# Performance work log

Hardware: AMD Instinct MI355X
Metric: run time of the kernel (lower is better)

Reference implementation:

```python
import jax, jax.numpy as jnp
import numpy as np

K = 9
BN_EPS = 1e-5
NEG_SLOPE = 0.2


def setup_inputs() -> dict:
    key = jax.random.key(0)
    ks = jax.random.split(key, 8)
    B, C, H, W = 16, 128, 32, 32
    s1 = 1.0 / np.sqrt(2 * C)
    s2 = 1.0 / np.sqrt(C)
    return {
        "x": jax.random.normal(ks[0], (B, C, H, W), dtype=jnp.float32),
        "W1": jax.random.uniform(ks[1], (2 * C, C), dtype=jnp.float32, minval=-s1, maxval=s1),
        "b1": jax.random.uniform(ks[2], (C,), dtype=jnp.float32, minval=-s1, maxval=s1),
        "W2": jax.random.uniform(ks[3], (C, C), dtype=jnp.float32, minval=-s2, maxval=s2),
        "b2": jax.random.uniform(ks[4], (C,), dtype=jnp.float32, minval=-s2, maxval=s2),
        "gamma": jnp.ones((C,), dtype=jnp.float32),
        "beta": jnp.zeros((C,), dtype=jnp.float32),
    }


def _leaky_relu(h):
    return jnp.where(h >= 0, h, NEG_SLOPE * h)


def reference(x, W1, b1, W2, b2, gamma, beta):
    B, C, H, W = x.shape
    N = H * W
    r = x
    feats = x.reshape(B, C, N).transpose(0, 2, 1)  # (B, N, C)

    # pairwise squared Euclidean distances (ordering identical to torch.cdist p=2)
    sq = jnp.sum(feats * feats, axis=-1)  # (B, N)
    d2 = sq[:, :, None] + sq[:, None, :] - 2.0 * jnp.einsum("bnc,bmc->bnm", feats, feats)
    _, idx = jax.lax.top_k(-d2, K)  # k smallest distances -> (B, N, K) int32

    neighbors = jax.vmap(lambda f, i: f[i])(feats, idx)  # (B, N, K, C)
    center = feats[:, :, None, :]  # (B, N, 1, C)
    edge = jnp.concatenate(
        [jnp.broadcast_to(center, neighbors.shape), neighbors - center], axis=-1
    )  # (B, N, K, 2C)

    h = _leaky_relu(edge @ W1 + b1)
    h = h @ W2 + b2  # (B, N, K, C)
    msg = jnp.max(h, axis=2)  # (B, N, C)

    out = msg.transpose(0, 2, 1).reshape(B, C, H, W)

    # BatchNorm2d (training mode: batch statistics, biased variance)
    mean = jnp.mean(out, axis=(0, 2, 3), keepdims=True)
    var = jnp.mean((out - mean) ** 2, axis=(0, 2, 3), keepdims=True)
    g = gamma.reshape(1, C, 1, 1)
    b = beta.reshape(1, C, 1, 1)
    out = g * (out - mean) * jax.lax.rsqrt(var + BN_EPS) + b

    return jax.nn.relu(out + r)
```

## Files before the change

### kernel.cpp

```cpp
#include <hip/hip_runtime.h>

#define B_ 16
#define C_ 128
#define N_ 1024
#define K_ 9
#define NEG_SLOPE 0.2f
#define BN_EPS 1e-5f

typedef __attribute__((ext_vector_type(8))) short short8;
typedef __attribute__((ext_vector_type(4))) float f32x4;
typedef __attribute__((ext_vector_type(4))) unsigned short u16x4;

__device__ __forceinline__ unsigned short f2bf(float f) {
    union { float f; unsigned u; } v; v.f = f;
    unsigned r = v.u + 0x7fffu + ((v.u >> 16) & 1u);
    return (unsigned short)(r >> 16);
}
__device__ __forceinline__ float bf2f(unsigned short h) {
    union { unsigned u; float f; } v; v.u = ((unsigned)h) << 16; return v.f;
}
__device__ __forceinline__ unsigned umin_(unsigned a, unsigned b) { return a < b ? a : b; }

__global__ __launch_bounds__(256) void k_transpose(const float* __restrict__ x,
                                                   float* __restrict__ featsT)
{
    __shared__ float t[32][33];
    int blk = blockIdx.x;
    int b = blk / 128;
    int rem = blk % 128;
    int c0 = (rem / 32) * 32;
    int n0 = (rem % 32) * 32;
    int tj = threadIdx.x & 31;
    int ti = threadIdx.x >> 5;
    #pragma unroll
    for (int s = 0; s < 32; s += 8)
        t[ti + s][tj] = x[(b * C_ + c0 + ti + s) * N_ + n0 + tj];
    __syncthreads();
    #pragma unroll
    for (int s = 0; s < 32; s += 8)
        featsT[(b * N_ + n0 + ti + s) * C_ + c0 + tj] = t[tj][ti + s];
}

__global__ __launch_bounds__(256) void k_prep(const float* __restrict__ featsT,
        unsigned short* __restrict__ Bf, float* __restrict__ sq)
{
    int tid = threadIdx.x;
    int lane = tid & 63, wv = tid >> 6;
    int half = lane >> 5;
    int l2 = lane & 31;
    int gp = blockIdx.x * 8 + wv * 2 + half;
    int b = gp >> 10, n = gp & 1023;

    int ch0 = (l2 & 15) * 8;
    const float4* f4 = (const float4*)&featsT[gp * C_ + ch0];
    float4 v0 = f4[0], v1 = f4[1];

    u16x4 o0, o1;
    if (l2 < 16) {
        o0.x = f2bf(v0.x); o0.y = f2bf(v0.y); o0.z = f2bf(v0.z); o0.w = f2bf(v0.w);
        o1.x = f2bf(v1.x); o1.y = f2bf(v1.y); o1.z = f2bf(v1.z); o1.w = f2bf(v1.w);
    } else {
        o0.x = f2bf(v0.x - bf2f(f2bf(v0.x))); o0.y = f2bf(v0.y - bf2f(f2bf(v0.y)));
        o0.z = f2bf(v0.z - bf2f(f2bf(v0.z))); o0.w = f2bf(v0.w - bf2f(f2bf(v0.w)));
        o1.x = f2bf(v1.x - bf2f(f2bf(v1.x))); o1.y = f2bf(v1.y - bf2f(f2bf(v1.y)));
        o1.z = f2bf(v1.z - bf2f(f2bf(v1.z))); o1.w = f2bf(v1.w - bf2f(f2bf(v1.w)));
    }
    long chunk = (((long)(b * 8 + (l2 >> 2)) * 64 + (n >> 4)) << 6) + ((l2 & 3) * 16 + (n & 15));
    *(u16x4*)&Bf[chunk * 8]     = o0;
    *(u16x4*)&Bf[chunk * 8 + 4] = o1;

    float ss = v0.x*v0.x + v0.y*v0.y + v0.z*v0.z + v0.w*v0.w
             + v1.x*v1.x + v1.y*v1.y + v1.z*v1.z + v1.w*v1.w;
    #pragma unroll
    for (int off = 1; off < 16; off <<= 1)
        ss += __shfl_xor(ss, off);
    if (l2 == 0) sq[gp] = ss;
}

#define STAGE_READ(PH, VARR) do {                                              \
    const int tl_ = (PH) >> 1, rb_ = ((PH) & 1) * 2;                           \
    _Pragma("unroll")                                                          \
    for (int t = 0; t < 8; ++t) {                                              \
        int col = ((wv * 8 + t) << 4) + cl;                                    \
        keybuf[quad * 2 + 0][col] = karr[tl_][t][rb_ + 0];                     \
        keybuf[quad * 2 + 1][col] = karr[tl_][t][rb_ + 1];                     \
    }                                                                          \
    __syncthreads();                                                           \
    _Pragma("unroll")                                                          \
    for (int j = 0; j < 16; ++j) VARR[j] = keybuf[wv][lane + (j << 6)];        \
    __syncthreads();                                                           \
} while (0)

#define TOP2_INIT(VARR, M1, M2, J1, J2) do {                                   \
    M1 = 0xFFFFFFFFu; M2 = 0xFFFFFFFFu; J1 = 0; J2 = 0;                        \
    _Pragma("unroll")                                                          \
    for (int j = 0; j < 16; ++j) {                                             \
        unsigned x_ = VARR[j], jc_ = (unsigned)j;                              \
        bool b1_ = x_ < M1, b2_ = x_ < M2;                                     \
        unsigned tk_ = b1_ ? M1 : x_, tj_ = b1_ ? J1 : jc_;                    \
        M2 = b2_ ? tk_ : M2; J2 = b2_ ? tj_ : J2;                              \
        M1 = b1_ ? x_ : M1; J1 = b1_ ? jc_ : J1;                               \
    }                                                                          \
} while (0)

#define ROW_ROUND(VARR, M1, M2, J1, J2, G, ROWPTR) do {                        \
    bool t_ = (M1 == (G));                                                     \
    unsigned long long bal_ = __ballot(t_);                                    \
    bool win_;                                                                 \
    if (__popcll(bal_) > 1) {               \
        unsigned mc_ = t_ ? (unsigned)(lane + (J1 << 6)) : 0xFFFFFFFFu;        \
        unsigned cm_ = mc_;                                                    \
        _Pragma("unroll")                                                      \
        for (int off = 1; off < 64; off <<= 1)                                 \
            cm_ = umin_(cm_, (unsigned)__shfl_xor((int)cm_, off));             \
        win_ = t_ && (mc_ == cm_);                   \
    } else {                                                                   \
        win_ = t_;                                                             \
    }                                                                          \
    if (win_) {                                                                \
        idxout[(ROWPTR) + q] = lane + (int)(J1 << 6);                          \
        unsigned gk_ = M1, gj_ = J1;                                           \
        M1 = M2; J1 = J2; M2 = 0xFFFFFFFFu;                                    \
        if (M1 == 0xFFFFFFFFu) {             \
            _Pragma("unroll")                                                  \
            for (int j = 0; j < 16; ++j) {                                     \
                unsigned x_ = VARR[j], jc_ = (unsigned)j;                      \
                bool dead_ = (x_ < gk_) || (x_ == gk_ && jc_ <= gj_);          \
                unsigned xk_ = dead_ ? 0xFFFFFFFFu : x_;                       \
                bool b1_ = xk_ < M1, b2_ = xk_ < M2;                           \
                unsigned tk_ = b1_ ? M1 : xk_, tj_ = b1_ ? J1 : jc_;           \
                M2 = b2_ ? tk_ : M2; J2 = b2_ ? tj_ : J2;                      \
                M1 = b1_ ? xk_ : M1; J1 = b1_ ? jc_ : J1;                      \
            }                                                                  \
        }                                                                      \
    }                                                                          \
} while (0)

__global__ __launch_bounds__(512, 4) void k_knn(
        const unsigned short* __restrict__ Bf, const float* __restrict__ sq,
        int* __restrict__ idxout)
{
    __shared__ unsigned keybuf[8][1028];
    __shared__ float sqn[32];

    int L = blockIdx.x;
    int xcd = L & 7, slot = L >> 3;
    int b = xcd * 2 + (slot >> 5);
    int tile32 = slot & 31;
    int n0 = tile32 * 32;
    int tid = threadIdx.x;

    if (tid < 32) sqn[tid] = sq[b * N_ + n0 + tid];
    __syncthreads();

    int wv = tid >> 6, lane = tid & 63, quad = lane >> 4, cl = lane & 15;

    f32x4 acc[2][8];
    #pragma unroll
    for (int tl = 0; tl < 2; ++tl)
        #pragma unroll
        for (int t = 0; t < 8; ++t) acc[tl][t] = (f32x4){0.f, 0.f, 0.f, 0.f};

    const short8* bfp = (const short8*)Bf;
    #pragma unroll
    for (int kb = 0; kb < 4; ++kb) {
        long ab0 = (((long)(b * 8 + kb) * 64 + tile32 * 2) << 6) + quad * 16 + cl;
        short8 afh0 = bfp[ab0];
        short8 afl0 = bfp[ab0 + 16384];
        short8 afh1 = bfp[ab0 + 64];
        short8 afl1 = bfp[ab0 + 16384 + 64];
        long bh = (((long)(b * 8 + kb) * 64 + wv * 8) << 6) + lane;
        long bl = bh + 16384;
        #pragma unroll
        for (int t = 0; t < 8; ++t) {
            short8 bfr = bfp[bh + t * 64];
            acc[0][t] = __builtin_amdgcn_mfma_f32_16x16x32_bf16(afh0, bfr, acc[0][t], 0, 0, 0);
            acc[0][t] = __builtin_amdgcn_mfma_f32_16x16x32_bf16(afl0, bfr, acc[0][t], 0, 0, 0);
            acc[1][t] = __builtin_amdgcn_mfma_f32_16x16x32_bf16(afh1, bfr, acc[1][t], 0, 0, 0);
            acc[1][t] = __builtin_amdgcn_mfma_f32_16x16x32_bf16(afl1, bfr, acc[1][t], 0, 0, 0);
        }
        #pragma unroll
        for (int t = 0; t < 8; ++t) {
            short8 bfr = bfp[bl + t * 64];
            acc[0][t] = __builtin_amdgcn_mfma_f32_16x16x32_bf16(afh0, bfr, acc[0][t], 0, 0, 0);
            acc[1][t] = __builtin_amdgcn_mfma_f32_16x16x32_bf16(afh1, bfr, acc[1][t], 0, 0, 0);
        }
    }

    float smc[8];
    #pragma unroll
    for (int t = 0; t < 8; ++t)
        smc[t] = sq[b * N_ + ((wv * 8 + t) << 4) + cl];

    unsigned karr[2][8][4];
    #pragma unroll
    for (int tl = 0; tl < 2; ++tl)
        #pragma unroll
        for (int t = 0; t < 8; ++t)
            #pragma unroll
            for (int r = 0; r < 4; ++r) {
                float d2 = fmaf(-2.f, acc[tl][t][r], smc[t] + sqn[tl * 16 + quad * 4 + r]);
                unsigned bits = __float_as_uint(d2);
                karr[tl][t][r] = bits ^ ((unsigned)((int)bits >> 31) | 0x80000000u);
            }

    unsigned vA[16], vB[16], vC[16], vD[16];
    STAGE_READ(0, vA);
    STAGE_READ(1, vB);
    STAGE_READ(2, vC);
    STAGE_READ(3, vD);

    int rbase = ((wv >> 1) << 2) + (wv & 1);
    int rowP0 = (b * N_ + n0 + rbase) * K_;
    int rowP1 = (b * N_ + n0 + rbase + 2) * K_;
    int rowP2 = (b * N_ + n0 + 16 + rbase) * K_;
    int rowP3 = (b * N_ + n0 + 16 + rbase + 2) * K_;

    unsigned mA1, mA2, jA1, jA2, mB1, mB2, jB1, jB2;
    unsigned mC1, mC2, jC1, jC2, mD1, mD2, jD1, jD2;
    TOP2_INIT(vA, mA1, mA2, jA1, jA2);
    TOP2_INIT(vB, mB1, mB2, jB1, jB2);
    TOP2_INIT(vC, mC1, mC2, jC1, jC2);
    TOP2_INIT(vD, mD1, mD2, jD1, jD2);

    #pragma unroll 1
    for (int q = 0; q < K_; ++q) {
        unsigned gA = mA1, gB = mB1, gC = mC1, gD = mD1;
        #pragma unroll
        for (int off = 1; off < 64; off <<= 1) {
            gA = umin_(gA, (unsigned)__shfl_xor((int)gA, off));
            gB = umin_(gB, (unsigned)__shfl_xor((int)gB, off));
            gC = umin_(gC, (unsigned)__shfl_xor((int)gC, off));
            gD = umin_(gD, (unsigned)__shfl_xor((int)gD, off));
        }
        ROW_ROUND(vA, mA1, mA2, jA1, jA2, gA, rowP0);
        ROW_ROUND(vB, mB1, mB2, jB1, jB2, gB, rowP1);
        ROW_ROUND(vC, mC1, mC2, jC1, jC2, gC, rowP2);
        ROW_ROUND(vD, mD1, mD2, jD1, jD2, gD, rowP3);
    }
}

__global__ __launch_bounds__(256) void k_prepack(const float* __restrict__ W1,
        const float* __restrict__ W2, unsigned short* __restrict__ wf1,
        unsigned short* __restrict__ wf2)
{
    int t = blockIdx.x * 256 + threadIdx.x;
    if (t < 4096) {
        int kk = t >> 9, w = (t >> 6) & 7, lane = t & 63;
        int quad = lane >> 4, col = lane & 15;
        #pragma unroll
        for (int j = 0; j < 8; ++j)
            wf1[t * 8 + j] = f2bf(W1[(kk * 32 + quad * 8 + j) * C_ + 16 * w + col]);
    } else if (t < 6144) {
        int t2 = t - 4096;
        int kk = t2 >> 9, w = (t2 >> 6) & 7, lane = t2 & 63;
        int quad = lane >> 4, col = lane & 15;
        #pragma unroll
        for (int j = 0; j < 8; ++j)
            wf2[t2 * 8 + j] = f2bf(W2[(kk * 32 + quad * 8 + j) * C_ + 16 * w + col]);
    }
}

__global__ __launch_bounds__(512, 6) void k_edge(const float* __restrict__ featsT,
        const int* __restrict__ idx, const unsigned short* __restrict__ wf1,
        const unsigned short* __restrict__ wf2, const float* __restrict__ b1,
        const float* __restrict__ b2, float* __restrict__ msg)
{
    __shared__ __align__(16) char smem[52224];
    unsigned short* diffs = (unsigned short*)smem;
    unsigned short* cenb  = (unsigned short*)(smem + 21760);
    unsigned short* h2b   = (unsigned short*)smem;
    unsigned short* h1    = (unsigned short*)(smem + 26112);
    unsigned short* ccb   = (unsigned short*)(smem + 47872);
    __shared__ int nb[72];

    int L = blockIdx.x;
    int xcd = L & 7, slot = L >> 3;
    int b = xcd * 2 + (slot >> 7);
    int tile = slot & 127;
    int n0 = tile * 8;
    int tid = threadIdx.x;

    if (tid < 72) nb[tid] = idx[(b * N_ + n0 + tid / 9) * K_ + tid % 9];
    __syncthreads();

    {
        int g = tid >> 6, j = tid & 63;
        int chunk = j & 31, ch = chunk << 2, half = j >> 5;
        const float4* fT4 = (const float4*)featsT;
        float4 cv = fT4[(b * N_ + n0 + g) * 32 + chunk];
        if (half == 0) {
            u16x4 cb; cb.x = f2bf(cv.x); cb.y = f2bf(cv.y);
            cb.z = f2bf(cv.z); cb.w = f2bf(cv.w);
            *(u16x4*)&cenb[g * 136 + ch] = cb;
        }
        int qb = half ? 5 : 0, qe = half ? 9 : 5;
        for (int q = qb; q < qe; ++q) {
            int e = g * 9 + q;
            float4 nv = fT4[(b * N_ + nb[e]) * 32 + chunk];
            u16x4 db;
            db.x = f2bf(nv.x - cv.x); db.y = f2bf(nv.y - cv.y);
            db.z = f2bf(nv.z - cv.z); db.w = f2bf(nv.w - cv.w);
            *(u16x4*)&diffs[e * 136 + ch] = db;
        }
    }
    __syncthreads();

    int wv = tid >> 6, lane = tid & 63;
    int quad = lane >> 4, cl = lane & 15;
    const short8* w1f = (const short8*)wf1;
    const short8* w2f = (const short8*)wf2;

    {
        float b1v = b1[16 * wv + cl];
        f32x4 a = (f32x4){b1v, b1v, b1v, b1v};
        #pragma unroll
        for (int kk = 0; kk < 4; ++kk) {
            short8 af = *(const short8*)&cenb[cl * 136 + kk * 32 + quad * 8];
            short8 bf = w1f[(kk * 8 + wv) * 64 + lane];
            a = __builtin_amdgcn_mfma_f32_16x16x32_bf16(af, bf, a, 0, 0, 0);
        }
        #pragma unroll
        for (int r = 0; r < 4; ++r)
            ccb[(quad * 4 + r) * 136 + 16 * wv + cl] = f2bf(a[r]);
    }

    #pragma unroll
    for (int t = 0; t < 5; ++t) {
        f32x4 a = (f32x4){0.f, 0.f, 0.f, 0.f};
        #pragma unroll
        for (int kb = 0; kb < 4; ++kb) {
            short8 af = *(const short8*)&diffs[(16 * t + cl) * 136 + kb * 32 + quad * 8];
            short8 bf = w1f[((kb + 4) * 8 + wv) * 64 + lane];
            a = __builtin_amdgcn_mfma_f32_16x16x32_bf16(af, bf, a, 0, 0, 0);
        }
        #pragma unroll
        for (int r = 0; r < 4; ++r) {
            int row = 16 * t + quad * 4 + r;
            int pt = row / 9; if (pt > 7) pt = 7;
            float v = a[r] + bf2f(ccb[pt * 136 + 16 * wv + cl]);
            v = (v >= 0.f) ? v : NEG_SLOPE * v;
            h1[row * 136 + 16 * wv + cl] = f2bf(v);
        }
    }
    __syncthreads();

    #pragma unroll
    for (int t = 0; t < 5; ++t) {
        f32x4 a = (f32x4){0.f, 0.f, 0.f, 0.f};
        #pragma unroll
        for (int kb = 0; kb < 4; ++kb) {
            short8 af = *(const short8*)&h1[(16 * t + cl) * 136 + kb * 32 + quad * 8];
            short8 bf = w2f[(kb * 8 + wv) * 64 + lane];
            a = __builtin_amdgcn_mfma_f32_16x16x32_bf16(af, bf, a, 0, 0, 0);
        }
        #pragma unroll
        for (int r = 0; r < 4; ++r)
            h2b[(16 * t + quad * 4 + r) * 136 + 16 * wv + cl] = f2bf(a[r]);
    }
    __syncthreads();

    int p = tid & 7, nb8 = tid >> 3;
    #pragma unroll
    for (int it = 0; it < 2; ++it) {
        int n = nb8 + 64 * it;
        float m = bf2f(h2b[(p * 9) * 136 + n]);
        #pragma unroll
        for (int q = 1; q < 9; ++q)
            m = fmaxf(m, bf2f(h2b[(p * 9 + q) * 136 + n]));
        msg[(b * C_ + n) * N_ + n0 + p] = m + b2[n];
    }
}

__global__ __launch_bounds__(256) void k_bnstats(const float* __restrict__ msg,
        const float* __restrict__ gamma, const float* __restrict__ beta,
        float* __restrict__ scale, float* __restrict__ shift)
{
    int c = blockIdx.x, tid = threadIdx.x;
    float s = 0.f, ss = 0.f;
    for (int b = 0; b < B_; ++b) {
        const float* row = msg + (b * C_ + c) * N_;
        for (int j = tid; j < N_; j += 256) {
            float v = row[j];
            s += v; ss += v * v;
        }
    }
    __shared__ float rs[256], rss[256];
    rs[tid] = s; rss[tid] = ss;
    __syncthreads();
    for (int off = 128; off > 0; off >>= 1) {
        if (tid < off) { rs[tid] += rs[tid + off]; rss[tid] += rss[tid + off]; }
        __syncthreads();
    }
    if (tid == 0) {
        float mean = rs[0] / (float)(B_ * N_);
        float var = rss[0] / (float)(B_ * N_) - mean * mean;
        float inv = 1.0f / sqrtf(var + BN_EPS);
        float g = gamma[c];
        scale[c] = g * inv;
        shift[c] = beta[c] - g * inv * mean;
    }
}

__global__ __launch_bounds__(256) void k_final(const float* __restrict__ msg,
        const float* __restrict__ x, const float* __restrict__ scale,
        const float* __restrict__ shift, float* __restrict__ out)
{
    int i = blockIdx.x * 256 + threadIdx.x;
    int e = i << 2;
    int c = (e >> 10) & 127;
    float sc = scale[c], sh = shift[c];
    float4 m4 = reinterpret_cast<const float4*>(msg)[i];
    float4 x4 = reinterpret_cast<const float4*>(x)[i];
    float4 o;
    o.x = fmaxf(m4.x * sc + sh + x4.x, 0.f);
    o.y = fmaxf(m4.y * sc + sh + x4.y, 0.f);
    o.z = fmaxf(m4.z * sc + sh + x4.z, 0.f);
    o.w = fmaxf(m4.w * sc + sh + x4.w, 0.f);
    reinterpret_cast<float4*>(out)[i] = o;
}

extern "C" void kernel_launch(void* const* d_in, const int* in_sizes, int n_in,
                              void* d_out, int out_size, void* d_ws, size_t ws_size,
                              hipStream_t stream)
{
    const float* x     = (const float*)d_in[0];
    const float* W1    = (const float*)d_in[1];
    const float* b1    = (const float*)d_in[2];
    const float* W2    = (const float*)d_in[3];
    const float* b2    = (const float*)d_in[4];
    const float* gamma = (const float*)d_in[5];
    const float* beta  = (const float*)d_in[6];
    float* out = (float*)d_out;

    float* ws     = (float*)d_ws;
    float* featsT = ws;
    float* msg    = ws + 2097152;
    unsigned short* Bf = (unsigned short*)(ws + 2097152);
    float* sq     = ws + 4194304;
    float* scale  = ws + 4210688;
    float* shift  = ws + 4210816;
    int*   idx    = (int*)(ws + 4210944);
    unsigned short* wf1 = (unsigned short*)(ws + 4358400);
    unsigned short* wf2 = (unsigned short*)(ws + 4374784);

    k_transpose<<<2048, 256, 0, stream>>>(x, featsT);
    k_prep     <<<2048, 256, 0, stream>>>(featsT, Bf, sq);
    k_prepack  <<<  24, 256, 0, stream>>>(W1, W2, wf1, wf2);
    k_knn      <<< 512, 512, 0, stream>>>(Bf, sq, idx);
    k_edge     <<<2048, 512, 0, stream>>>(featsT, idx, wf1, wf2, b1, b2, msg);
    k_bnstats  <<< 128, 256, 0, stream>>>(msg, gamma, beta, scale, shift);
    k_final    <<<2048, 256, 0, stream>>>(msg, x, scale, shift, out);
}
```

Baseline: 159.8 us.

## Fuse transpose, prep and weight prepack into one staging kernel; vectorize BN stats

Merges the transpose, bf16 split/sq-norm prep and weight prepack kernels into a single k_stage launch that keeps a 128x32 tile in shared memory, avoiding a global round trip through featsT for the prep step and two launches. In k_edge, weight fragments for each GEMM are hoisted into registers once instead of being reloaded per row tile. k_bnstats switches to float4 loads with fully unrolled accumulation. The staging kernel uses far fewer blocks with larger shared memory, which reduces parallelism for that phase, and the hoisted weights add register pressure.

Result: faster. 142.0 us (-11.1%).

```diff
diff --git a/kernel.cpp b/kernel.cpp
--- a/kernel.cpp
+++ b/kernel.cpp
@@ -21,60 +21,89 @@
 }
 __device__ __forceinline__ unsigned umin_(unsigned a, unsigned b) { return a < b ? a : b; }
 
-__global__ __launch_bounds__(256) void k_transpose(const float* __restrict__ x,
-                                                   float* __restrict__ featsT)
-{
-    __shared__ float t[32][33];
+__global__ __launch_bounds__(256) void k_stage(const float* __restrict__ x,
+        const float* __restrict__ W1, const float* __restrict__ W2,
+        float* __restrict__ featsT, unsigned short* __restrict__ Bf,
+        float* __restrict__ sq, unsigned short* __restrict__ wf1,
+        unsigned short* __restrict__ wf2)
+{
     int blk = blockIdx.x;
-    int b = blk / 128;
-    int rem = blk % 128;
-    int c0 = (rem / 32) * 32;
-    int n0 = (rem % 32) * 32;
-    int tj = threadIdx.x & 31;
-    int ti = threadIdx.x >> 5;
-    #pragma unroll
-    for (int s = 0; s < 32; s += 8)
-        t[ti + s][tj] = x[(b * C_ + c0 + ti + s) * N_ + n0 + tj];
-    __syncthreads();
-    #pragma unroll
-    for (int s = 0; s < 32; s += 8)
-        featsT[(b * N_ + n0 + ti + s) * C_ + c0 + tj] = t[tj][ti + s];
-}
-
-__global__ __launch_bounds__(256) void k_prep(const float* __restrict__ featsT,
-        unsigned short* __restrict__ Bf, float* __restrict__ sq)
-{
     int tid = threadIdx.x;
+
+    if (blk >= 512) {
+        int t = (blk - 512) * 256 + tid;
+        if (t < 4096) {
+            int kk = t >> 9, w = (t >> 6) & 7, lane = t & 63;
+            int quad = lane >> 4, col = lane & 15;
+            #pragma unroll
+            for (int j = 0; j < 8; ++j)
+                wf1[t * 8 + j] = f2bf(W1[(kk * 32 + quad * 8 + j) * C_ + 16 * w + col]);
+        } else {
+            int t2 = t - 4096;
+            int kk = t2 >> 9, w = (t2 >> 6) & 7, lane = t2 & 63;
+            int quad = lane >> 4, col = lane & 15;
+            #pragma unroll
+            for (int j = 0; j < 8; ++j)
+                wf2[t2 * 8 + j] = f2bf(W2[(kk * 32 + quad * 8 + j) * C_ + 16 * w + col]);
+        }
+        return;
+    }
+
+    __shared__ float tch[128][33];
+    int b = blk >> 5;
+    int n0 = (blk & 31) * 32;
+
+    const float4* xv = (const float4*)x;
+    #pragma unroll
+    for (int pass = 0; pass < 4; ++pass) {
+        int c = pass * 32 + (tid >> 3);
+        int f = tid & 7;
+        float4 v = xv[(b * C_ + c) * 256 + (n0 >> 2) + f];
+        tch[c][f * 4 + 0] = v.x; tch[c][f * 4 + 1] = v.y;
+        tch[c][f * 4 + 2] = v.z; tch[c][f * 4 + 3] = v.w;
+    }
+    __syncthreads();
+
+    #pragma unroll
+    for (int pass = 0; pass < 16; ++pass) {
+        int li = pass * 256 + tid;
+        int p = li >> 7, c = li & 127;
+        featsT[(b * N_ + n0 + p) * C_ + c] = tch[c][p];
+    }
+
     int lane = tid & 63, wv = tid >> 6;
-    int half = lane >> 5;
-    int l2 = lane & 31;
-    int gp = blockIdx.x * 8 + wv * 2 + half;
-    int b = gp >> 10, n = gp & 1023;
-
+    int half = lane >> 5, l2 = lane & 31;
     int ch0 = (l2 & 15) * 8;
-    const float4* f4 = (const float4*)&featsT[gp * C_ + ch0];
-    float4 v0 = f4[0], v1 = f4[1];
-
-    u16x4 o0, o1;
-    if (l2 < 16) {
-        o0.x = f2bf(v0.x); o0.y = f2bf(v0.y); o0.z = f2bf(v0.z); o0.w = f2bf(v0.w);
-        o1.x = f2bf(v1.x); o1.y = f2bf(v1.y); o1.z = f2bf(v1.z); o1.w = f2bf(v1.w);
-    } else {
-        o0.x = f2bf(v0.x - bf2f(f2bf(v0.x))); o0.y = f2bf(v0.y - bf2f(f2bf(v0.y)));
-        o0.z = f2bf(v0.z - bf2f(f2bf(v0.z))); o0.w = f2bf(v0.w - bf2f(f2bf(v0.w)));
-        o1.x = f2bf(v1.x - bf2f(f2bf(v1.x))); o1.y = f2bf(v1.y - bf2f(f2bf(v1.y)));
-        o1.z = f2bf(v1.z - bf2f(f2bf(v1.z))); o1.w = f2bf(v1.w - bf2f(f2bf(v1.w)));
-    }
-    long chunk = (((long)(b * 8 + (l2 >> 2)) * 64 + (n >> 4)) << 6) + ((l2 & 3) * 16 + (n & 15));
-    *(u16x4*)&Bf[chunk * 8]     = o0;
-    *(u16x4*)&Bf[chunk * 8 + 4] = o1;
-
-    float ss = v0.x*v0.x + v0.y*v0.y + v0.z*v0.z + v0.w*v0.w
-             + v1.x*v1.x + v1.y*v1.y + v1.z*v1.z + v1.w*v1.w;
-    #pragma unroll
-    for (int off = 1; off < 16; off <<= 1)
-        ss += __shfl_xor(ss, off);
-    if (l2 == 0) sq[gp] = ss;
+    #pragma unroll
+    for (int sub = 0; sub < 4; ++sub) {
+        int pl = sub * 8 + wv * 2 + half;
+        int n = n0 + pl;
+        float a0 = tch[ch0 + 0][pl], a1 = tch[ch0 + 1][pl];
+        float a2 = tch[ch0 + 2][pl], a3 = tch[ch0 + 3][pl];
+        float a4 = tch[ch0 + 4][pl], a5 = tch[ch0 + 5][pl];
+        float a6 = tch[ch0 + 6][pl], a7 = tch[ch0 + 7][pl];
+
+        u16x4 o0, o1;
+        if (l2 < 16) {
+            o0.x = f2bf(a0); o0.y = f2bf(a1); o0.z = f2bf(a2); o0.w = f2bf(a3);
+            o1.x = f2bf(a4); o1.y = f2bf(a5); o1.z = f2bf(a6); o1.w = f2bf(a7);
+        } else {
+            o0.x = f2bf(a0 - bf2f(f2bf(a0))); o0.y = f2bf(a1 - bf2f(f2bf(a1)));
+            o0.z = f2bf(a2 - bf2f(f2bf(a2))); o0.w = f2bf(a3 - bf2f(f2bf(a3)));
+            o1.x = f2bf(a4 - bf2f(f2bf(a4))); o1.y = f2bf(a5 - bf2f(f2bf(a5)));
+            o1.z = f2bf(a6 - bf2f(f2bf(a6))); o1.w = f2bf(a7 - bf2f(f2bf(a7)));
+        }
+        long chunk = (((long)(b * 8 + (l2 >> 2)) * 64 + (n >> 4)) << 6)
+                   + ((l2 & 3) * 16 + (n & 15));
+        *(u16x4*)&Bf[chunk * 8]     = o0;
+        *(u16x4*)&Bf[chunk * 8 + 4] = o1;
+
+        float ss = a0*a0 + a1*a1 + a2*a2 + a3*a3 + a4*a4 + a5*a5 + a6*a6 + a7*a7;
+        #pragma unroll
+        for (int off = 1; off < 16; off <<= 1)
+            ss += __shfl_xor(ss, off);
+        if (l2 == 0) sq[b * N_ + n] = ss;
+    }
 }
 
 #define STAGE_READ(PH, VARR) do {                                              \
@@ -240,27 +269,6 @@
     }
 }
 
-__global__ __launch_bounds__(256) void k_prepack(const float* __restrict__ W1,
-        const float* __restrict__ W2, unsigned short* __restrict__ wf1,
-        unsigned short* __restrict__ wf2)
-{
-    int t = blockIdx.x * 256 + threadIdx.x;
-    if (t < 4096) {
-        int kk = t >> 9, w = (t >> 6) & 7, lane = t & 63;
-        int quad = lane >> 4, col = lane & 15;
-        #pragma unroll
-        for (int j = 0; j < 8; ++j)
-            wf1[t * 8 + j] = f2bf(W1[(kk * 32 + quad * 8 + j) * C_ + 16 * w + col]);
-    } else if (t < 6144) {
-        int t2 = t - 4096;
-        int kk = t2 >> 9, w = (t2 >> 6) & 7, lane = t2 & 63;
-        int quad = lane >> 4, col = lane & 15;
-        #pragma unroll
-        for (int j = 0; j < 8; ++j)
-            wf2[t2 * 8 + j] = f2bf(W2[(kk * 32 + quad * 8 + j) * C_ + 16 * w + col]);
-    }
-}
-
 __global__ __launch_bounds__(512, 6) void k_edge(const float* __restrict__ featsT,
         const int* __restrict__ idx, const unsigned short* __restrict__ wf1,
         const unsigned short* __restrict__ wf2, const float* __restrict__ b1,
@@ -325,38 +333,48 @@
             ccb[(quad * 4 + r) * 136 + 16 * wv + cl] = f2bf(a[r]);
     }
 
-    #pragma unroll
-    for (int t = 0; t < 5; ++t) {
-        f32x4 a = (f32x4){0.f, 0.f, 0.f, 0.f};
-        #pragma unroll
-        for (int kb = 0; kb < 4; ++kb) {
-            short8 af = *(const short8*)&diffs[(16 * t + cl) * 136 + kb * 32 + quad * 8];
-            short8 bf = w1f[((kb + 4) * 8 + wv) * 64 + lane];
-            a = __builtin_amdgcn_mfma_f32_16x16x32_bf16(af, bf, a, 0, 0, 0);
-        }
-        #pragma unroll
-        for (int r = 0; r < 4; ++r) {
-            int row = 16 * t + quad * 4 + r;
-            int pt = row / 9; if (pt > 7) pt = 7;
-            float v = a[r] + bf2f(ccb[pt * 136 + 16 * wv + cl]);
-            v = (v >= 0.f) ? v : NEG_SLOPE * v;
-            h1[row * 136 + 16 * wv + cl] = f2bf(v);
-        }
-    }
-    __syncthreads();
-
-    #pragma unroll
-    for (int t = 0; t < 5; ++t) {
-        f32x4 a = (f32x4){0.f, 0.f, 0.f, 0.f};
-        #pragma unroll
-        for (int kb = 0; kb < 4; ++kb) {
-            short8 af = *(const short8*)&h1[(16 * t + cl) * 136 + kb * 32 + quad * 8];
-            short8 bf = w2f[(kb * 8 + wv) * 64 + lane];
-            a = __builtin_amdgcn_mfma_f32_16x16x32_bf16(af, bf, a, 0, 0, 0);
-        }
-        #pragma unroll
-        for (int r = 0; r < 4; ++r)
-            h2b[(16 * t + quad * 4 + r) * 136 + 16 * wv + cl] = f2bf(a[r]);
+    {
+        short8 wb[4];
+        #pragma unroll
+        for (int kb = 0; kb < 4; ++kb)
+            wb[kb] = w1f[((kb + 4) * 8 + wv) * 64 + lane];
+        #pragma unroll
+        for (int t = 0; t < 5; ++t) {
+            f32x4 a = (f32x4){0.f, 0.f, 0.f, 0.f};
+            #pragma unroll
+            for (int kb = 0; kb < 4; ++kb) {
+                short8 af = *(const short8*)&diffs[(16 * t + cl) * 136 + kb * 32 + quad * 8];
+                a = __builtin_amdgcn_mfma_f32_16x16x32_bf16(af, wb[kb], a, 0, 0, 0);
+            }
+            #pragma unroll
+            for (int r = 0; r < 4; ++r) {
+                int row = 16 * t + quad * 4 + r;
+                int pt = row / 9; if (pt > 7) pt = 7;
+                float v = a[r] + bf2f(ccb[pt * 136 + 16 * wv + cl]);
+                v = (v >= 0.f) ? v : NEG_SLOPE * v;
+                h1[row * 136 + 16 * wv + cl] = f2bf(v);
+            }
+        }
+    }
+    __syncthreads();
+
+    {
+        short8 wb[4];
+        #pragma unroll
+        for (int kb = 0; kb < 4; ++kb)
+            wb[kb] = w2f[(kb * 8 + wv) * 64 + lane];
+        #pragma unroll
+        for (int t = 0; t < 5; ++t) {
+            f32x4 a = (f32x4){0.f, 0.f, 0.f, 0.f};
+            #pragma unroll
+            for (int kb = 0; kb < 4; ++kb) {
+                short8 af = *(const short8*)&h1[(16 * t + cl) * 136 + kb * 32 + quad * 8];
+                a = __builtin_amdgcn_mfma_f32_16x16x32_bf16(af, wb[kb], a, 0, 0, 0);
+            }
+            #pragma unroll
+            for (int r = 0; r < 4; ++r)
+                h2b[(16 * t + quad * 4 + r) * 136 + 16 * wv + cl] = f2bf(a[r]);
+        }
     }
     __syncthreads();
 
@@ -377,14 +395,17 @@
         float* __restrict__ scale, float* __restrict__ shift)
 {
     int c = blockIdx.x, tid = threadIdx.x;
-    float s = 0.f, ss = 0.f;
+    const float4* m4 = (const float4*)msg;
+    float4 s4 = {0.f, 0.f, 0.f, 0.f}, ss4 = {0.f, 0.f, 0.f, 0.f};
+    #pragma unroll
     for (int b = 0; b < B_; ++b) {
-        const float* row = msg + (b * C_ + c) * N_;
-        for (int j = tid; j < N_; j += 256) {
-            float v = row[j];
-            s += v; ss += v * v;
-        }
-    }
+        float4 v = m4[(b * C_ + c) * 256 + tid];
+        s4.x += v.x; s4.y += v.y; s4.z += v.z; s4.w += v.w;
+        ss4.x += v.x * v.x; ss4.y += v.y * v.y;
+        ss4.z += v.z * v.z; ss4.w += v.w * v.w;
+    }
+    float s = (s4.x + s4.y) + (s4.z + s4.w);
+    float ss = (ss4.x + ss4.y) + (ss4.z + ss4.w);
     __shared__ float rs[256], rss[256];
     rs[tid] = s; rss[tid] = ss;
     __syncthreads();
@@ -444,11 +465,9 @@
     unsigned short* wf1 = (unsigned short*)(ws + 4358400);
     unsigned short* wf2 = (unsigned short*)(ws + 4374784);
 
-    k_transpose<<<2048, 256, 0, stream>>>(x, featsT);
-    k_prep     <<<2048, 256, 0, stream>>>(featsT, Bf, sq);
-    k_prepack  <<<  24, 256, 0, stream>>>(W1, W2, wf1, wf2);
-    k_knn      <<< 512, 512, 0, stream>>>(Bf, sq, idx);
-    k_edge     <<<2048, 512, 0, stream>>>(featsT, idx, wf1, wf2, b1, b2, msg);
-    k_bnstats  <<< 128, 256, 0, stream>>>(msg, gamma, beta, scale, shift);
-    k_final    <<<2048, 256, 0, stream>>>(msg, x, scale, shift, out);
-}
+    k_stage  <<< 536, 256, 0, stream>>>(x, W1, W2, featsT, Bf, sq, wf1, wf2);
+    k_knn    <<< 512, 512, 0, stream>>>(Bf, sq, idx);
+    k_edge   <<<2048, 512, 0, stream>>>(featsT, idx, wf1, wf2, b1, b2, msg);
+    k_bnstats<<< 128, 256, 0, stream>>>(msg, gamma, beta, scale, shift);
+    k_final  <<<2048, 256, 0, stream>>>(msg, x, scale, shift, out);
+}
```
